# Performance work log

Hardware: AMD Instinct MI355X
Metric: run time of the kernel (lower is better)

Reference implementation:

```python
import jax, jax.numpy as jnp
import numpy as np

DT = 1.0 / 120.0  # hard-coded in the original SystemModel / EKF
N_TRAJ, T = 2048, 512
COV = np.array([2.5e-07, 2.5e-07, 0.0091, 2e-10, 1e-07, 0.01, 0.1], dtype=np.float32)


def _dynamics(s, friction, damping):
    # 6-dim puck state: [x, y, dx, dy, theta, dtheta]
    # Table damping (linear drag) + friction (smoothed Coulomb) act on linear velocity,
    # matching the SystemModel(tableDamping, tableFriction, dt=1/120) free-motion step.
    x, y, dx, dy, th, dth = s
    dx2 = dx - DT * (damping * dx + friction * jnp.tanh(100.0 * dx))
    dy2 = dy - DT * (damping * dy + friction * jnp.tanh(100.0 * dy))
    return jnp.stack([x + DT * dx, y + DT * dy, dx2, dy2, th + DT * dth, dth])


def _ekf_losses(measurements, init_state, dyna_params, Q, R, P0):
    friction, damping = dyna_params[0], dyna_params[1]
    dt_ = measurements.dtype
    H = jnp.zeros((3, 6), dt_).at[0, 0].set(1.0).at[1, 1].set(1.0).at[2, 4].set(1.0)
    I6 = jnp.eye(6, dtype=dt_)
    f = lambda s: _dynamics(s, friction, damping)
    Jf = jax.jacfwd(f)

    def step(carry, z):
        s, P = carry
        # --- predict ---
        s_pred = f(s)
        F = Jf(s)                      # 6x6 Jacobian of dynamics
        P_pred = F @ P @ F.T + Q
        # --- update ---
        y = z - H @ s_pred             # 3-dim innovation
        S = H @ P_pred @ H.T + R       # 3x3 innovation covariance
        S_inv = jnp.linalg.inv(S)
        K = P_pred @ H.T @ S_inv       # 6x3 Kalman gain
        s_new = s_pred + K @ y
        P_new = (I6 - K @ H) @ P_pred
        # per-point loss: det(S) (via slogdet as in the original) + Mahalanobis term
        sign, logdet = jnp.linalg.slogdet(S)
        loss = sign * jnp.exp(logdet) + y @ S_inv @ y
        return (s_new, P_new), loss

    def run(z_seq, s0):
        _, losses = jax.lax.scan(step, (s0, P0), z_seq)
        return losses

    return jax.vmap(run)(measurements, init_state).reshape(-1)


def setup_inputs() -> dict:
    key = jax.random.key(0)
    k1, k2 = jax.random.split(key, 2)
    measurements = jax.random.normal(k1, (N_TRAJ, T, 3), dtype=jnp.float32)
    init_state = jax.random.normal(k2, (N_TRAJ, 6), dtype=jnp.float32)
    # dyna_params = [tableFriction, tableDamping, restitution, rimFriction]
    dyna_params = jnp.array([0.1, 0.3, 0.8, 0.1], dtype=jnp.float32)
    cov = jnp.asarray(COV)
    R = jnp.diag(cov[:3])
    Q = jnp.diag(jnp.array([cov[3], cov[3], cov[4], cov[4], cov[5], cov[6]], dtype=jnp.float32))
    P0 = jnp.eye(6, dtype=jnp.float32) * 0.01
    return {"measurements": measurements, "init_state": init_state,
            "dyna_params": dyna_params, "Q": Q, "R": R, "P0": P0}


def reference(measurements, init_state, dyna_params, Q, R, P0):
    return _ekf_losses(measurements, init_state, dyna_params, Q, R, P0)
```

## Files before the change

### kernel.cpp

```cpp
#include <hip/hip_runtime.h>
#include <math.h>


#define TRIPLES 21
#define TILE    32
#define ZS      100
#define ZBUFSZ  (TRIPLES * ZS)
#define SMS     35
#define CHUNKS_Z 504

__device__ __forceinline__ float frcp(float x) { return __builtin_amdgcn_rcpf(x); }

__device__ __forceinline__ float tanh100(float v) {
    float e = exp2f(288.53900817779268f * v);
    return fmaf(-2.0f, frcp(e + 1.0f), 1.0f);
}

__global__ __launch_bounds__(64, 1) void ekf_kernel(
    const float* __restrict__ meas,
    const float* __restrict__ init_state,
    const float* __restrict__ dyna,
    const float* __restrict__ Qm,
    const float* __restrict__ Rm,
    const float* __restrict__ P0m,
    float* __restrict__ out,
    int n_traj, int T)
{
    __shared__ float  zbuf[2 * ZBUFSZ];
    __shared__ float2 sSM[64 * SMS];

    const int lane  = threadIdx.x;
    const int k     = lane / 3;
    const int j     = lane - 3 * k;
    const int traj0 = blockIdx.x * TRIPLES;
    const int kk    = (k < TRIPLES) ? k : (TRIPLES - 1);
    const int traj  = traj0 + kk;
    const int traj_eff = (traj < n_traj) ? traj : (n_traj - 1);

    const int NT = T / TILE;
    const int T3 = 3 * T;

    const float DTc  = 1.0f / 120.0f;
    const float fric = dyna[0], damp = dyna[1];
    const bool  lin  = (j == 2);
    const float ca_l  = lin ? 1.0f : (1.0f - DTc * damp);
    const float cf_l  = lin ? 0.0f : (DTc * fric);
    const float cb_l  = 100.0f * cf_l;
    const float ca2_l = ca_l - cb_l;
    const int pi = (j == 0) ? 0 : (j == 1) ? 1 : 4;
    const int vi = pi + 2;
    const float qp = Qm[pi * 7], qv = Qm[vi * 7], qc = Qm[pi * 6 + vi];
    const float r  = Rm[j * 4];
    float p00 = P0m[pi * 7], p02 = P0m[pi * 6 + vi], p22 = P0m[vi * 7];
    float pos = init_state[traj_eff * 6 + pi];
    float vel = init_state[traj_eff * 6 + vi];

    int gofs[8], lofs[8];
    #pragma unroll
    for (int rr = 0; rr < 8; ++rr) {
        int c = rr * 64 + lane;
        c = (c < CHUNKS_Z) ? c : (CHUNKS_Z - 1);
        int ck = c / 24;
        int cw = c - 24 * ck;
        int tr = traj0 + ck; tr = (tr < n_traj) ? tr : (n_traj - 1);
        gofs[rr] = tr * T3 + 4 * cw;
        lofs[rr] = ck * ZS + 4 * cw;
    }

    const int fhi  = lane >> 5;
    const int ftw  = lane & 31;
    const int fsm0 = 3 * fhi * SMS + ftw;
    const int fob0 = (traj0 + fhi) * T + ftw;

    float4 g[8];
    #pragma unroll
    for (int rr = 0; rr < 8; ++rr)
        g[rr] = *(const float4*)(meas + (size_t)gofs[rr]);

    int cur = 0;

    #pragma unroll 1
    for (int tile = 0; tile < NT; ++tile) {
        const int zo = cur * ZBUFSZ;
        #pragma unroll
        for (int rr = 0; rr < 8; ++rr)
            *(float4*)&zbuf[zo + lofs[rr]] = g[rr];

        const int ntile = (tile + 1 < NT) ? (tile + 1) : tile;
        const int nofs  = ntile * (TILE * 3);
        #pragma unroll
        for (int rr = 0; rr < 8; ++rr)
            g[rr] = *(const float4*)(meas + (size_t)(gofs[rr] + nofs));

        const float* __restrict__ zr = &zbuf[zo + kk * ZS + j];
        float zv[TILE];
        #pragma unroll
        for (int tl = 0; tl < TILE; ++tl) zv[tl] = zr[3 * tl];

        float Sv[TILE], Mv[TILE];
        #pragma unroll
        for (int tl = 0; tl < TILE; ++tl) {
            const float z    = zv[tl];
            const float tx   = tanh100(vel);
            const float u    = fmaf(DTc, p22, p02);
            const float pp00 = fmaf(DTc, p02 + u, p00) + qp;
            const float a    = fmaf(cb_l, tx * tx, ca2_l);
            const float pp02 = fmaf(a, u, qc);
            const float pp22 = fmaf(a * p22, a, qv);
            const float sp   = fmaf(DTc, vel, pos);
            const float sv   = fmaf(-cf_l, tx, ca_l * vel);
            const float S    = pp00 + r;
            const float rs   = frcp(S);
            const float yv   = z - sp;
            const float rsy  = rs * yv;
            pos = fmaf(pp00, rsy, sp);
            vel = fmaf(pp02, rsy, sv);
            const float gg = r * rs;
            const float K1 = pp02 * rs;
            p00 = pp00 * gg;
            p02 = pp02 * gg;
            p22 = fmaf(-K1, pp02, pp22);
            Sv[tl] = S;
            Mv[tl] = (yv * yv) * rs;
        }

        float2* __restrict__ smr = &sSM[lane * SMS];
        #pragma unroll
        for (int tl = 0; tl < TILE; ++tl)
            smr[tl] = make_float2(Sv[tl], Mv[tl]);

        const int tb = tile * TILE;
        #pragma unroll
        for (int rr = 0; rr < 11; ++rr) {
            const int ck = 2 * rr + fhi;
            const bool ok = (rr * 64 + lane < TRIPLES * TILE) &&
                            (traj0 + ck < n_traj);
            const int sa = fsm0 + rr * (6 * SMS);
            const float2 a0 = sSM[sa];
            const float2 a1 = sSM[sa + SMS];
            const float2 a2 = sSM[sa + 2 * SMS];
            const float loss = (a0.x * a1.x) * a2.x + (a0.y + a1.y + a2.y);
            if (ok) out[(size_t)(fob0 + 2 * rr * T + tb)] = loss;
        }

        cur ^= 1;
    }
}

extern "C" void kernel_launch(void* const* d_in, const int* in_sizes, int n_in,
                              void* d_out, int out_size, void* d_ws, size_t ws_size,
                              hipStream_t stream) {
    const float* meas = (const float*)d_in[0];
    const float* init_state = (const float*)d_in[1];
    const float* dyna = (const float*)d_in[2];
    const float* Qm  = (const float*)d_in[3];
    const float* Rm  = (const float*)d_in[4];
    const float* P0m = (const float*)d_in[5];
    float* out = (float*)d_out;

    const int n_traj = in_sizes[1] / 6;
    const int T = in_sizes[0] / (n_traj * 3);

    const int grid = (n_traj + TRIPLES - 1) / TRIPLES;
    ekf_kernel<<<grid, 64, 0, stream>>>(meas, init_state, dyna, Qm, Rm, P0m,
                                        out, n_traj, T);
}
```

Baseline: 125.9 us.

## Load measurements directly per lane with register double-buffering and shorten recurrence

```diff
diff --git a/kernel.cpp b/kernel.cpp
--- a/kernel.cpp
+++ b/kernel.cpp
@@ -4,17 +4,9 @@
 
 #define TRIPLES 21
 #define TILE    32
-#define ZS      100
-#define ZBUFSZ  (TRIPLES * ZS)
 #define SMS     35
-#define CHUNKS_Z 504
 
 __device__ __forceinline__ float frcp(float x) { return __builtin_amdgcn_rcpf(x); }
-
-__device__ __forceinline__ float tanh100(float v) {
-    float e = exp2f(288.53900817779268f * v);
-    return fmaf(-2.0f, frcp(e + 1.0f), 1.0f);
-}
 
 __global__ __launch_bounds__(64, 1) void ekf_kernel(
     const float* __restrict__ meas,
@@ -26,8 +18,7 @@
     float* __restrict__ out,
     int n_traj, int T)
 {
-    __shared__ float  zbuf[2 * ZBUFSZ];
-    __shared__ float2 sSM[64 * SMS];
+    __shared__ float2 sSM[66 * SMS];
 
     const int lane  = threadIdx.x;
     const int k     = lane / 3;
@@ -40,111 +31,105 @@
     const int NT = T / TILE;
     const int T3 = 3 * T;
 
-    const float DTc  = 1.0f / 120.0f;
+    const float DTc = 1.0f / 120.0f;
+    const float Cc  = 288.53900817779268f;
     const float fric = dyna[0], damp = dyna[1];
-    const bool  lin  = (j == 2);
-    const float ca_l  = lin ? 1.0f : (1.0f - DTc * damp);
-    const float cf_l  = lin ? 0.0f : (DTc * fric);
-    const float cb_l  = 100.0f * cf_l;
-    const float ca2_l = ca_l - cb_l;
+    const bool  lin = (j == 2);
+    const float ca  = lin ? 1.0f : (1.0f - DTc * damp);
+    const float cf  = lin ? 0.0f : (DTc * fric);
+    const float cb  = 100.0f * cf;
+    const float ca2 = ca - cb;
     const int pi = (j == 0) ? 0 : (j == 1) ? 1 : 4;
     const int vi = pi + 2;
     const float qp = Qm[pi * 7], qv = Qm[vi * 7], qc = Qm[pi * 6 + vi];
-    const float r  = Rm[j * 4];
-    float p00 = P0m[pi * 7], p02 = P0m[pi * 6 + vi], p22 = P0m[vi * 7];
+    const float r   = Rm[j * 4];
+    const float nr2 = -r * r;
+    const float w0  = r + r + qp;
+    float p02 = P0m[pi * 6 + vi], p22 = P0m[vi * 7];
+    float w   = P0m[pi * 7] + qp + r;
     float pos = init_state[traj_eff * 6 + pi];
     float vel = init_state[traj_eff * 6 + vi];
-
-    int gofs[8], lofs[8];
-    #pragma unroll
-    for (int rr = 0; rr < 8; ++rr) {
-        int c = rr * 64 + lane;
-        c = (c < CHUNKS_Z) ? c : (CHUNKS_Z - 1);
-        int ck = c / 24;
-        int cw = c - 24 * ck;
-        int tr = traj0 + ck; tr = (tr < n_traj) ? tr : (n_traj - 1);
-        gofs[rr] = tr * T3 + 4 * cw;
-        lofs[rr] = ck * ZS + 4 * cw;
-    }
 
     const int fhi  = lane >> 5;
     const int ftw  = lane & 31;
     const int fsm0 = 3 * fhi * SMS + ftw;
     const int fob0 = (traj0 + fhi) * T + ftw;
 
-    float4 g[8];
+    const float* __restrict__ zlane = meas + (size_t)traj_eff * T3 + j;
+
+    float zA[TILE], zB[TILE];
     #pragma unroll
-    for (int rr = 0; rr < 8; ++rr)
-        g[rr] = *(const float4*)(meas + (size_t)gofs[rr]);
+    for (int tl = 0; tl < TILE; ++tl) zA[tl] = zlane[3 * tl];
 
-    int cur = 0;
+#define EKF_PHASE(ZC, ZN, TIDX)                                              \
+    do {                                                                     \
+        const int tile_ = (TIDX);                                            \
+        const int nt_   = (tile_ + 1 < NT) ? (tile_ + 1) : tile_;            \
+        const float* __restrict__ znp_ = zlane + 96 * nt_;                   \
+        _Pragma("unroll")                                                    \
+        for (int tl = 0; tl < TILE; ++tl) ZN[tl] = znp_[3 * tl];             \
+        float Sv[TILE], Mv[TILE];                                            \
+        _Pragma("unroll")                                                    \
+        for (int tl = 0; tl < TILE; ++tl) {                                  \
+            const float z    = ZC[tl];                                       \
+            const float e    = exp2f(Cc * vel);                              \
+            const float ie   = frcp(e + 1.0f);                               \
+            const float tx   = fmaf(-2.0f, ie, 1.0f);                        \
+            const float t2   = tx * tx;                                      \
+            const float u    = fmaf(DTc, p22, p02);                          \
+            const float pu   = p02 + u;                                      \
+            const float S    = fmaf(DTc, pu, w);             \
+            const float rs   = frcp(S);                                      \
+            const float sp   = fmaf(DTc, vel, pos);                          \
+            const float yv   = z - sp;                                       \
+            const float rsy  = rs * yv;                                      \
+            const float cbu  = cb * u;                                       \
+            const float b02  = fmaf(ca2, u, qc);                             \
+            const float pp02 = fmaf(cbu, t2, b02);                           \
+            const float a    = fmaf(cb, t2, ca2);                            \
+            const float ap   = a * p22;                                      \
+            const float pp22 = fmaf(ap, a, qv);                              \
+            const float sv   = fmaf(-cf, tx, ca * vel);                      \
+            vel = fmaf(pp02, rsy, sv);                                       \
+            const float pp00 = S - r;                                        \
+            pos = fmaf(pp00, rsy, sp);                                       \
+            w   = fmaf(nr2, rs, w0);                                         \
+            const float gg   = r * rs;                                       \
+            p02 = pp02 * gg;                                                 \
+            const float k1   = pp02 * rs;                                    \
+            p22 = fmaf(-k1, pp02, pp22);                                     \
+            Sv[tl] = S;                                                      \
+            Mv[tl] = yv * rsy;                                               \
+        }                                                                    \
+              \
+        float2* __restrict__ smr_ = &sSM[lane * SMS];                        \
+        _Pragma("unroll")                                                    \
+        for (int tl = 0; tl < TILE; ++tl)                                    \
+            smr_[tl] = make_float2(Sv[tl], Mv[tl]);                          \
+                \
+        const int tb_ = tile_ * TILE;                                        \
+        _Pragma("unroll")                                                    \
+        for (int rr = 0; rr < 11; ++rr) {                                    \
+            const int ck_ = 2 * rr + fhi;                                    \
+            const bool ok_ = (rr * 64 + lane < TRIPLES * TILE) &&            \
+                             (traj0 + ck_ < n_traj);                         \
+            const int sa_ = fsm0 + rr * (6 * SMS);                           \
+            const float2 a0_ = sSM[sa_];                                     \
+            const float2 a1_ = sSM[sa_ + SMS];                               \
+            const float2 a2_ = sSM[sa_ + 2 * SMS];                           \
+            const float loss_ = (a0_.x * a1_.x) * a2_.x +                    \
+                                (a0_.y + a1_.y + a2_.y);                     \
+            if (ok_) out[(size_t)(fob0 + 2 * rr * T + tb_)] = loss_;         \
+        }                                                                    \
+    } while (0)
 
     #pragma unroll 1
-    for (int tile = 0; tile < NT; ++tile) {
-        const int zo = cur * ZBUFSZ;
-        #pragma unroll
-        for (int rr = 0; rr < 8; ++rr)
-            *(float4*)&zbuf[zo + lofs[rr]] = g[rr];
+    for (int th = 0; th < NT; th += 2) {
+        EKF_PHASE(zA, zB, th);
+        if (th + 1 < NT) EKF_PHASE(zB, zA, th + 1);
+    }
 
-        const int ntile = (tile + 1 < NT) ? (tile + 1) : tile;
-        const int nofs  = ntile * (TILE * 3);
-        #pragma unroll
-        for (int rr = 0; rr < 8; ++rr)
-            g[rr] = *(const float4*)(meas + (size_t)(gofs[rr] + nofs));
-
-        const float* __restrict__ zr = &zbuf[zo + kk * ZS + j];
-        float zv[TILE];
-        #pragma unroll
-        for (int tl = 0; tl < TILE; ++tl) zv[tl] = zr[3 * tl];
-
-        float Sv[TILE], Mv[TILE];
-        #pragma unroll
-        for (int tl = 0; tl < TILE; ++tl) {
-            const float z    = zv[tl];
-            const float tx   = tanh100(vel);
-            const float u    = fmaf(DTc, p22, p02);
-            const float pp00 = fmaf(DTc, p02 + u, p00) + qp;
-            const float a    = fmaf(cb_l, tx * tx, ca2_l);
-            const float pp02 = fmaf(a, u, qc);
-            const float pp22 = fmaf(a * p22, a, qv);
-            const float sp   = fmaf(DTc, vel, pos);
-            const float sv   = fmaf(-cf_l, tx, ca_l * vel);
-            const float S    = pp00 + r;
-            const float rs   = frcp(S);
-            const float yv   = z - sp;
-            const float rsy  = rs * yv;
-            pos = fmaf(pp00, rsy, sp);
-            vel = fmaf(pp02, rsy, sv);
-            const float gg = r * rs;
-            const float K1 = pp02 * rs;
-            p00 = pp00 * gg;
-            p02 = pp02 * gg;
-            p22 = fmaf(-K1, pp02, pp22);
-            Sv[tl] = S;
-            Mv[tl] = (yv * yv) * rs;
-        }
-
-        float2* __restrict__ smr = &sSM[lane * SMS];
-        #pragma unroll
-        for (int tl = 0; tl < TILE; ++tl)
-            smr[tl] = make_float2(Sv[tl], Mv[tl]);
-
-        const int tb = tile * TILE;
-        #pragma unroll
-        for (int rr = 0; rr < 11; ++rr) {
-            const int ck = 2 * rr + fhi;
-            const bool ok = (rr * 64 + lane < TRIPLES * TILE) &&
-                            (traj0 + ck < n_traj);
-            const int sa = fsm0 + rr * (6 * SMS);
-            const float2 a0 = sSM[sa];
-            const float2 a1 = sSM[sa + SMS];
-            const float2 a2 = sSM[sa + 2 * SMS];
-            const float loss = (a0.x * a1.x) * a2.x + (a0.y + a1.y + a2.y);
-            if (ok) out[(size_t)(fob0 + 2 * rr * T + tb)] = loss;
-        }
-
-        cur ^= 1;
-    }
+#undef EKF_PHASE
 }
 
 extern "C" void kernel_launch(void* const* d_in, const int* in_sizes, int n_in,
```

New measurement: 120.8 us. -4.0%, faster.
